# Kernel tuning notes

Measured on AMD Instinct MI355X. Metric: run time of the kernel, lower is better.

## Reference

```python
import jax, jax.numpy as jnp
import numpy as np

N = 50000       # num entities (nodes)
E = 800000      # num edges
R = 200         # num relation types
DIN = 64        # dim_in_ent
DREL = 64       # dim_rel
DOUT = 64       # dim_out_ent
H = 8           # num_head
DH = DOUT // H  # dim_hid_ent
EPS = 1e-6


def setup_inputs() -> dict:
    key = jax.random.key(0)
    ks = jax.random.split(key, 8)
    return {
        "emb_ent": jax.random.normal(ks[0], (N, DIN), dtype=jnp.float32),
        "emb_rel": jax.random.normal(ks[1], (R, DREL), dtype=jnp.float32),
        "attn_W": jax.random.normal(ks[2], (DOUT, 2 * DIN + DREL), dtype=jnp.float32) * 0.05,
        "attn_b": jnp.zeros((DOUT,), dtype=jnp.float32),
        "attn_vec": jax.random.normal(ks[3], (1, H, DH), dtype=jnp.float32) * 0.05,
        "aggr_W": jax.random.normal(ks[4], (DOUT, DIN + DREL), dtype=jnp.float32) * 0.05,
        "aggr_b": jnp.zeros((DOUT,), dtype=jnp.float32),
        "head_idxs": jax.random.randint(ks[5], (E,), 0, N),
        "tail_idxs": jax.random.randint(ks[6], (E,), 0, N),
        "rel_idxs": jax.random.randint(ks[7], (E,), 0, R),
    }


def reference(emb_ent, emb_rel, attn_W, attn_b, attn_vec, aggr_W, aggr_b,
              head_idxs, tail_idxs, rel_idxs):
    num_ent = emb_ent.shape[0]
    # per-node in-degree and mean incoming relation embedding (self relation)
    ones = jnp.ones(tail_idxs.shape[0], dtype=emb_ent.dtype)
    ent_freq = jax.ops.segment_sum(ones, tail_idxs, num_segments=num_ent)[:, None]
    rel_e = emb_rel[rel_idxs]                                             # [E, DREL]
    self_rel = jax.ops.segment_sum(rel_e, tail_idxs, num_segments=num_ent) / (ent_freq + EPS)
    # append self-loops: every node gets a self edge carrying self_rel
    emb_rels = jnp.concatenate([rel_e, self_rel], axis=0)                 # [E+N, DREL]
    sl = jnp.arange(num_ent)
    h_idx = jnp.concatenate([head_idxs, sl], axis=0)                      # [M]
    t_idx = jnp.concatenate([tail_idxs, sl], axis=0)                      # [M]
    # attention logits per edge per head
    cat_att = jnp.concatenate([emb_ent[t_idx], emb_ent[h_idx], emb_rels], axis=-1)  # [M, 2*DIN+DREL]
    a = jax.nn.leaky_relu(cat_att @ attn_W.T + attn_b, negative_slope=0.2)
    a = a.reshape(-1, H, DH)
    raw = jnp.sum(a * attn_vec, axis=-1)                                  # [M, H]
    # per-destination-node multi-head softmax (stable, segment-wise)
    mx = jax.ops.segment_max(raw, t_idx, num_segments=num_ent)            # [num_ent, H]
    mx = jnp.where(jnp.isfinite(mx), mx, jnp.zeros_like(mx))              # empty segments -> 0 (matches torch init)
    av = jnp.exp(raw - mx[t_idx])                                         # [M, H]
    sums = jax.ops.segment_sum(av, t_idx, num_segments=num_ent)           # [num_ent, H]
    beta = av / (sums[t_idx] + EPS)                                       # [M, H]
    # message projection and weighted scatter-add aggregation
    cat = jnp.concatenate([emb_ent[h_idx], emb_rels], axis=-1)            # [M, DIN+DREL]
    aggr = (cat @ aggr_W.T + aggr_b).reshape(-1, H, DH)                   # [M, H, DH]
    out = jax.ops.segment_sum(beta[..., None] * aggr, t_idx, num_segments=num_ent)  # [num_ent, H, DH]
    return out.reshape(num_ent, H * DH)
```

## Files before the change

### kernel.cpp

```cpp
#include <hip/hip_runtime.h>
#include <math.h>

#define EPS 1e-6f

typedef _Float16 half2v __attribute__((ext_vector_type(2)));

__device__ __forceinline__ unsigned f2bf(float x) {
    unsigned u = __float_as_uint(x);
    return (u + 0x7FFFu + ((u >> 16) & 1u)) >> 16;
}

__device__ __forceinline__ float dpp_add_xor1(float t) {
    int u = __builtin_amdgcn_update_dpp(0, __float_as_int(t), 0xB1, 0xF, 0xF, true);
    return t + __int_as_float(u);
}
__device__ __forceinline__ float dpp_add_xor2(float t) {
    int u = __builtin_amdgcn_update_dpp(0, __float_as_int(t), 0x4E, 0xF, 0xF, true);
    return t + __int_as_float(u);
}
__device__ __forceinline__ float dpp_add_mirr8(float t) {
    int u = __builtin_amdgcn_update_dpp(0, __float_as_int(t), 0x141, 0xF, 0xF, true);
    return t + __int_as_float(u);
}

__device__ __forceinline__ float fdot2u(unsigned a, unsigned b, float c) {
    return __builtin_amdgcn_fdot2(__builtin_bit_cast(half2v, a),
                                  __builtin_bit_cast(half2v, b), c, false);
}
__device__ __forceinline__ unsigned pk16(float x, float y) {
    return __builtin_bit_cast(unsigned, __builtin_amdgcn_cvt_pkrtz(x, y));
}

__global__ __launch_bounds__(256) void tables_hist(
    const float* __restrict__ A, int M,
    const float* __restrict__ Ar, int Mr,
    const float* __restrict__ attn_W,
    const float* __restrict__ aggr_W,
    const float* __restrict__ attn_b, const float* __restrict__ aggr_b,
    float* __restrict__ Pt,
    unsigned short* __restrict__ PQh2,
    unsigned short* __restrict__ PQr2,
    const int* __restrict__ tail, int E, int* __restrict__ deg,
    int gN, int gr)
{
    __shared__ alignas(16) unsigned short As16[64][72];
    __shared__ alignas(16) unsigned short Ws16[64][72];
    const int tid = threadIdx.x;
    const int bid = (int)blockIdx.x;
    const int nEnt = 3 * gN;
    const int nRel = 2 * gr;

    if (bid < nEnt + nRel) {
        int slice, rt, Mrows;
        const float* Asrc;
        if (bid < nEnt) { slice = bid / gN;     rt = bid % gN; Asrc = A;  Mrows = M;  }
        else { int b2 = bid - nEnt; slice = 3 + b2 / gr; rt = b2 % gr; Asrc = Ar; Mrows = Mr; }
        const int r0 = rt * 64;

        for (int t = tid; t < 1024; t += 256) {
            int r = t >> 4, c4 = (t & 15) << 2;
            float4 v = make_float4(0.f, 0.f, 0.f, 0.f);
            if (r0 + r < Mrows)
                v = *reinterpret_cast<const float4*>(Asrc + (size_t)(r0 + r) * 64 + c4);
            *reinterpret_cast<uint2*>(&As16[r][c4]) =
                make_uint2(pk16(v.x, v.y), pk16(v.z, v.w));
        }
        const float* Wsrc; int ldw, koff;
        switch (slice) {
        case 0:  Wsrc = attn_W; ldw = 192; koff = 0;   break;
        case 1:  Wsrc = attn_W; ldw = 192; koff = 64;  break;
        case 2:  Wsrc = aggr_W; ldw = 128; koff = 0;   break;
        case 3:  Wsrc = attn_W; ldw = 192; koff = 128; break;
        default: Wsrc = aggr_W; ldw = 128; koff = 64;  break;
        }
        for (int t = tid; t < 1024; t += 256) {
            int c = t >> 4, k4 = (t & 15) << 2;
            float4 v = *reinterpret_cast<const float4*>(
                Wsrc + (size_t)c * ldw + koff + k4);
            *reinterpret_cast<uint2*>(&Ws16[c][k4]) =
                make_uint2(pk16(v.x, v.y), pk16(v.z, v.w));
        }
        __syncthreads();

        const int ti = tid >> 4, tj = tid & 15;
        float acc[4][4];
#pragma unroll
        for (int i = 0; i < 4; ++i)
#pragma unroll
            for (int j = 0; j < 4; ++j) acc[i][j] = 0.f;

#pragma unroll
        for (int k = 0; k < 64; k += 8) {
            uint4 a8[4], w8[4];
#pragma unroll
            for (int i = 0; i < 4; ++i)
                a8[i] = *reinterpret_cast<const uint4*>(&As16[ti + 16 * i][k]);
#pragma unroll
            for (int j = 0; j < 4; ++j)
                w8[j] = *reinterpret_cast<const uint4*>(&Ws16[tj + 16 * j][k]);
#pragma unroll
            for (int i = 0; i < 4; ++i)
#pragma unroll
                for (int j = 0; j < 4; ++j) {
                    float c0 = acc[i][j];
                    c0 = fdot2u(a8[i].x, w8[j].x, c0);
                    c0 = fdot2u(a8[i].y, w8[j].y, c0);
                    c0 = fdot2u(a8[i].z, w8[j].z, c0);
                    c0 = fdot2u(a8[i].w, w8[j].w, c0);
                    acc[i][j] = c0;
                }
        }

        if (slice == 0) {
#pragma unroll
            for (int i = 0; i < 4; ++i) {
                int r = r0 + ti + 16 * i;
                if (r < M)
#pragma unroll
                    for (int j = 0; j < 4; ++j)
                        Pt[(size_t)r * 64 + tj + 16 * j] = acc[i][j];
            }
        } else if (slice == 1) {
#pragma unroll
            for (int i = 0; i < 4; ++i) {
                int r = r0 + ti + 16 * i;
                if (r < M)
#pragma unroll
                    for (int j = 0; j < 4; ++j) {
                        int c = tj + 16 * j;
                        PQh2[((size_t)r * 64 + c) * 2 + 0] =
                            (unsigned short)f2bf(acc[i][j] + attn_b[c]);
                    }
            }
        } else if (slice == 2) {
#pragma unroll
            for (int i = 0; i < 4; ++i) {
                int r = r0 + ti + 16 * i;
                if (r < M)
#pragma unroll
                    for (int j = 0; j < 4; ++j) {
                        int c = tj + 16 * j;
                        PQh2[((size_t)r * 64 + c) * 2 + 1] =
                            (unsigned short)f2bf(acc[i][j] + aggr_b[c]);
                    }
            }
        } else if (slice == 3) {
#pragma unroll
            for (int i = 0; i < 4; ++i) {
                int r = r0 + ti + 16 * i;
                if (r < Mr)
#pragma unroll
                    for (int j = 0; j < 4; ++j)
                        PQr2[((size_t)r * 64 + tj + 16 * j) * 2 + 0] =
                            (unsigned short)f2bf(acc[i][j]);
            }
        } else {
#pragma unroll
            for (int i = 0; i < 4; ++i) {
                int r = r0 + ti + 16 * i;
                if (r < Mr)
#pragma unroll
                    for (int j = 0; j < 4; ++j)
                        PQr2[((size_t)r * 64 + tj + 16 * j) * 2 + 1] =
                            (unsigned short)f2bf(acc[i][j]);
            }
        }
    } else {
        const int base = ((bid - nEnt - nRel) * 256 + tid) * 4;
        if (base + 4 <= E) {
            int4 t4 = *reinterpret_cast<const int4*>(tail + base);
            atomicAdd(&deg[t4.x], 1);
            atomicAdd(&deg[t4.y], 1);
            atomicAdd(&deg[t4.z], 1);
            atomicAdd(&deg[t4.w], 1);
        } else {
            for (int k = 0; k < 4; ++k)
                if (base + k < E) atomicAdd(&deg[tail[base + k]], 1);
        }
    }
}

__global__ __launch_bounds__(256) void scan_chunk(const int* __restrict__ deg, int n,
                                                  int* __restrict__ incl, int* __restrict__ bsums)
{
    __shared__ int s[256];
    int tid = threadIdx.x;
    int i = blockIdx.x * 256 + tid;
    int v = (i < n) ? deg[i] : 0;
    int acc = v;
    s[tid] = acc;
    __syncthreads();
#pragma unroll
    for (int off = 1; off < 256; off <<= 1) {
        int add = (tid >= off) ? s[tid - off] : 0;
        __syncthreads();
        acc += add;
        s[tid] = acc;
        __syncthreads();
    }
    if (i < n) incl[i] = acc;
    if (tid == 255) bsums[blockIdx.x] = acc;
}

__global__ __launch_bounds__(256) void scan_final2(const int* __restrict__ deg,
                                                   const int* __restrict__ incl,
                                                   const int* __restrict__ bsums, int n,
                                                   int* __restrict__ offs,
                                                   int* __restrict__ cursor)
{
    __shared__ int s[256];
    const int tid = threadIdx.x;
    int partial = 0;
    for (int i = tid; i < (int)blockIdx.x; i += 256) partial += bsums[i];
    s[tid] = partial;
    __syncthreads();
#pragma unroll
    for (int off = 128; off > 0; off >>= 1) {
        if (tid < off) s[tid] += s[tid + off];
        __syncthreads();
    }
    const int base = s[0];
    int i = blockIdx.x * 256 + tid;
    if (i < n) {
        int e = incl[i] - deg[i] + base;
        offs[i] = e;
        cursor[i] = e;
    }
}

__global__ __launch_bounds__(256) void place_kernel(const int* __restrict__ head,
                                                    const int* __restrict__ tail,
                                                    const int* __restrict__ rel, int E,
                                                    int* __restrict__ cursor,
                                                    unsigned int* __restrict__ shr)
{
    const int base = (blockIdx.x * 256 + threadIdx.x) * 4;
    if (base + 4 <= E) {
        int4 h = *reinterpret_cast<const int4*>(head + base);
        int4 t = *reinterpret_cast<const int4*>(tail + base);
        int4 r = *reinterpret_cast<const int4*>(rel + base);
        int p;
        p = atomicAdd(&cursor[t.x], 1); shr[p] = ((unsigned)h.x << 8) | (unsigned)r.x;
        p = atomicAdd(&cursor[t.y], 1); shr[p] = ((unsigned)h.y << 8) | (unsigned)r.y;
        p = atomicAdd(&cursor[t.z], 1); shr[p] = ((unsigned)h.z << 8) | (unsigned)r.z;
        p = atomicAdd(&cursor[t.w], 1); shr[p] = ((unsigned)h.w << 8) | (unsigned)r.w;
    } else {
        for (int k = 0; k < 4; ++k) {
            int e = base + k;
            if (e < E) {
                int p = atomicAdd(&cursor[tail[e]], 1);
                shr[p] = ((unsigned)head[e] << 8) | (unsigned)rel[e];
            }
        }
    }
}

__global__ __launch_bounds__(256) void ingram_main(
    const float* __restrict__ Pt,
    const unsigned* __restrict__ PQh,
    const unsigned* __restrict__ PQr,
    const int* __restrict__ deg, const int* __restrict__ off,
    const unsigned* __restrict__ shr,
    const float* __restrict__ attn_vec,
    float* __restrict__ out, int N)
{
    const int lane = threadIdx.x & 63;
    const int node = blockIdx.x * 4 + (threadIdx.x >> 6);
    if (node >= N) return;

    const float vec = attn_vec[lane];
    const float ptd = Pt[(size_t)node * 64 + lane];
    const char* HBc = (const char*)PQh;
    const char* RBc = (const char*)PQr;
    const unsigned loff4 = (unsigned)lane << 2;

    const int start = __builtin_amdgcn_readfirstlane(off[node]);
    const int dg    = __builtin_amdgcn_readfirstlane(deg[node]);

    float S = 0.f, O = 0.f, SP = 0.f, SQ = 0.f;

    const int ng = (dg + 7) >> 3;
    unsigned Ah[8], Ar8[8], Bh[8], Br8[8];

#define LOADG(gbase, H, R)                                                   \
    {                                                                        \
        _Pragma("unroll")                                                    \
        for (int k = 0; k < 8; ++k) {                                        \
            int idx = (gbase) + k;                                           \
            int e   = start + ((idx < dg) ? idx : (dg - 1));                 \
            unsigned p = shr[e];            \
            H[k] = *(const unsigned*)(HBc + (p & 0xFFFFFF00u) + loff4);      \
            R[k] = *(const unsigned*)(RBc + ((p & 255u) << 8) + loff4);      \
        }                                                                    \
    }

#define COMPUTE(gbase, H, R)                                                 \
    {                                                                        \
        _Pragma("unroll")                                                    \
        for (int k = 0; k < 8; ++k) {                                        \
            const int idx = (gbase) + k;                                     \
            const float valid = (idx < dg) ? 1.f : 0.f;                      \
            unsigned hb = H[k], rb = R[k];                                   \
            float hx = __uint_as_float(hb << 16);                            \
            float hy = __uint_as_float(hb & 0xFFFF0000u);                    \
            float rx = __uint_as_float(rb << 16);                            \
            float ry = __uint_as_float(rb & 0xFFFF0000u);                    \
            SP = fmaf(rx, valid, SP);                                        \
            SQ = fmaf(ry, valid, SQ);                                        \
            float pre = ptd + hx + rx;                                       \
            float a   = fmaxf(pre, 0.2f * pre);                              \
            float t   = a * vec;                                             \
            t = dpp_add_xor1(t);                                             \
            t = dpp_add_xor2(t);                                             \
            t = dpp_add_mirr8(t);                                            \
            float av = __expf(t) * valid;                                    \
            S += av;                                                         \
            O = fmaf(av, hy + ry, O);                                        \
        }                                                                    \
    }

    if (ng > 0) LOADG(0, Ah, Ar8);
    for (int g = 0; g < ng; g += 2) {
        if (g + 1 < ng) LOADG((g + 1) * 8, Bh, Br8);
        COMPUTE(g * 8, Ah, Ar8);
        if (g + 1 < ng) {
            if (g + 2 < ng) LOADG((g + 2) * 8, Ah, Ar8);
            COMPUTE((g + 1) * 8, Bh, Br8);
        }
    }
#undef LOADG
#undef COMPUTE

    {
        const float inv = 1.f / ((float)dg + EPS);
        unsigned hb = *(const unsigned*)(HBc + ((unsigned)node << 8) + loff4);
        float hx = __uint_as_float(hb << 16);
        float hy = __uint_as_float(hb & 0xFFFF0000u);
        float pre = ptd + hx + SP * inv;
        float a   = fmaxf(pre, 0.2f * pre);
        float t   = a * vec;
        t = dpp_add_xor1(t);
        t = dpp_add_xor2(t);
        t = dpp_add_mirr8(t);
        float av = __expf(t);
        S += av;
        O = fmaf(av, hy + SQ * inv, O);
    }

    out[(size_t)node * 64 + lane] = O / (S + EPS);
}

extern "C" void kernel_launch(void* const* d_in, const int* in_sizes, int n_in,
                              void* d_out, int out_size, void* d_ws, size_t ws_size,
                              hipStream_t stream)
{
    const float* emb_ent  = (const float*)d_in[0];
    const float* emb_rel  = (const float*)d_in[1];
    const float* attn_W   = (const float*)d_in[2];
    const float* attn_b   = (const float*)d_in[3];
    const float* attn_vec = (const float*)d_in[4];
    const float* aggr_W   = (const float*)d_in[5];
    const float* aggr_b   = (const float*)d_in[6];
    const int*   head     = (const int*)d_in[7];
    const int*   tail     = (const int*)d_in[8];
    const int*   rel      = (const int*)d_in[9];

    const int N = in_sizes[0] / 64;
    const int R = in_sizes[1] / 64;
    const int E = in_sizes[7];

    char* w = (char*)d_ws;
    float*    Pt  = (float*)w;        w += (size_t)N * 64 * sizeof(float);
    unsigned* PQh = (unsigned*)w;     w += (size_t)N * 64 * sizeof(unsigned);
    unsigned* PQr = (unsigned*)w;     w += (size_t)R * 64 * sizeof(unsigned);
    int* deg    = (int*)w;            w += (size_t)N * sizeof(int);
    int* incl   = (int*)w;            w += (size_t)N * sizeof(int);
    int* offs   = (int*)w;            w += (size_t)N * sizeof(int);
    int* cursor = (int*)w;            w += (size_t)N * sizeof(int);
    int* bsums  = (int*)w;            w += 256 * sizeof(int);
    unsigned int* shr = (unsigned int*)w;  w += (size_t)E * sizeof(unsigned int);

    hipMemsetAsync(deg, 0, (size_t)N * sizeof(int), stream);

    int gN = (N + 63) / 64;
    int gr = (R + 63) / 64;
    int gH = (E + 1023) / 1024;
    tables_hist<<<3 * gN + 2 * gr + gH, 256, 0, stream>>>(
        emb_ent, N, emb_rel, R, attn_W, aggr_W, attn_b, aggr_b,
        Pt, (unsigned short*)PQh, (unsigned short*)PQr,
        tail, E, deg, gN, gr);

    int nb = (N + 255) / 256;
    scan_chunk<<<nb, 256, 0, stream>>>(deg, N, incl, bsums);
    scan_final2<<<nb, 256, 0, stream>>>(deg, incl, bsums, N, offs, cursor);
    place_kernel<<<(E + 1023) / 1024, 256, 0, stream>>>(head, tail, rel, E, cursor, shr);

    ingram_main<<<(N + 3) / 4, 256, 0, stream>>>(Pt, PQh, PQr, deg, offs, shr,
                                                 attn_vec, (float*)d_out, N);
}
```

Baseline: 156.8 us.

## Fuse CSR construction into one cooperative kernel with grid-wide syncs

Replaces the memset, histogram, two scan kernels and placement kernel with a single cooperative kernel that zeroes degrees, builds the histogram, scans and places edges, separated by grid.sync barriers. The scan now has each block sum all preceding degrees directly instead of using a block-sums pass. The table GEMM moves into its own kernel and no longer overlaps with the histogram. This removes several launch gaps. In exchange it adds grid-barrier cost, a redundant O(N) prefix read per block, and a cooperative launch that requires all 2048 blocks to be co-resident.

```diff
diff --git a/kernel.cpp b/kernel.cpp
--- a/kernel.cpp
+++ b/kernel.cpp
@@ -1,5 +1,8 @@
 #include <hip/hip_runtime.h>
+#include <hip/hip_cooperative_groups.h>
 #include <math.h>
+
+namespace cg = cooperative_groups;
 
 #define EPS 1e-6f
 
@@ -31,142 +34,23 @@
     return __builtin_bit_cast(unsigned, __builtin_amdgcn_cvt_pkrtz(x, y));
 }
 
-__global__ __launch_bounds__(256) void tables_hist(
-    const float* __restrict__ A, int M,
-    const float* __restrict__ Ar, int Mr,
-    const float* __restrict__ attn_W,
-    const float* __restrict__ aggr_W,
-    const float* __restrict__ attn_b, const float* __restrict__ aggr_b,
-    float* __restrict__ Pt,
-    unsigned short* __restrict__ PQh2,
-    unsigned short* __restrict__ PQr2,
-    const int* __restrict__ tail, int E, int* __restrict__ deg,
-    int gN, int gr)
+__global__ __launch_bounds__(256) void csr_coop(
+    const int* __restrict__ head, const int* __restrict__ tail,
+    const int* __restrict__ rel, int E, int N,
+    int* __restrict__ deg, int* __restrict__ offs,
+    int* __restrict__ cursor, unsigned* __restrict__ shr)
 {
-    __shared__ alignas(16) unsigned short As16[64][72];
-    __shared__ alignas(16) unsigned short Ws16[64][72];
-    const int tid = threadIdx.x;
-    const int bid = (int)blockIdx.x;
-    const int nEnt = 3 * gN;
-    const int nRel = 2 * gr;
-
-    if (bid < nEnt + nRel) {
-        int slice, rt, Mrows;
-        const float* Asrc;
-        if (bid < nEnt) { slice = bid / gN;     rt = bid % gN; Asrc = A;  Mrows = M;  }
-        else { int b2 = bid - nEnt; slice = 3 + b2 / gr; rt = b2 % gr; Asrc = Ar; Mrows = Mr; }
-        const int r0 = rt * 64;
-
-        for (int t = tid; t < 1024; t += 256) {
-            int r = t >> 4, c4 = (t & 15) << 2;
-            float4 v = make_float4(0.f, 0.f, 0.f, 0.f);
-            if (r0 + r < Mrows)
-                v = *reinterpret_cast<const float4*>(Asrc + (size_t)(r0 + r) * 64 + c4);
-            *reinterpret_cast<uint2*>(&As16[r][c4]) =
-                make_uint2(pk16(v.x, v.y), pk16(v.z, v.w));
-        }
-        const float* Wsrc; int ldw, koff;
-        switch (slice) {
-        case 0:  Wsrc = attn_W; ldw = 192; koff = 0;   break;
-        case 1:  Wsrc = attn_W; ldw = 192; koff = 64;  break;
-        case 2:  Wsrc = aggr_W; ldw = 128; koff = 0;   break;
-        case 3:  Wsrc = attn_W; ldw = 192; koff = 128; break;
-        default: Wsrc = aggr_W; ldw = 128; koff = 64;  break;
-        }
-        for (int t = tid; t < 1024; t += 256) {
-            int c = t >> 4, k4 = (t & 15) << 2;
-            float4 v = *reinterpret_cast<const float4*>(
-                Wsrc + (size_t)c * ldw + koff + k4);
-            *reinterpret_cast<uint2*>(&Ws16[c][k4]) =
-                make_uint2(pk16(v.x, v.y), pk16(v.z, v.w));
-        }
-        __syncthreads();
-
-        const int ti = tid >> 4, tj = tid & 15;
-        float acc[4][4];
-#pragma unroll
-        for (int i = 0; i < 4; ++i)
-#pragma unroll
-            for (int j = 0; j < 4; ++j) acc[i][j] = 0.f;
-
-#pragma unroll
-        for (int k = 0; k < 64; k += 8) {
-            uint4 a8[4], w8[4];
-#pragma unroll
-            for (int i = 0; i < 4; ++i)
-                a8[i] = *reinterpret_cast<const uint4*>(&As16[ti + 16 * i][k]);
-#pragma unroll
-            for (int j = 0; j < 4; ++j)
-                w8[j] = *reinterpret_cast<const uint4*>(&Ws16[tj + 16 * j][k]);
-#pragma unroll
-            for (int i = 0; i < 4; ++i)
-#pragma unroll
-                for (int j = 0; j < 4; ++j) {
-                    float c0 = acc[i][j];
-                    c0 = fdot2u(a8[i].x, w8[j].x, c0);
-                    c0 = fdot2u(a8[i].y, w8[j].y, c0);
-                    c0 = fdot2u(a8[i].z, w8[j].z, c0);
-                    c0 = fdot2u(a8[i].w, w8[j].w, c0);
-                    acc[i][j] = c0;
-                }
-        }
-
-        if (slice == 0) {
-#pragma unroll
-            for (int i = 0; i < 4; ++i) {
-                int r = r0 + ti + 16 * i;
-                if (r < M)
-#pragma unroll
-                    for (int j = 0; j < 4; ++j)
-                        Pt[(size_t)r * 64 + tj + 16 * j] = acc[i][j];
-            }
-        } else if (slice == 1) {
-#pragma unroll
-            for (int i = 0; i < 4; ++i) {
-                int r = r0 + ti + 16 * i;
-                if (r < M)
-#pragma unroll
-                    for (int j = 0; j < 4; ++j) {
-                        int c = tj + 16 * j;
-                        PQh2[((size_t)r * 64 + c) * 2 + 0] =
-                            (unsigned short)f2bf(acc[i][j] + attn_b[c]);
-                    }
-            }
-        } else if (slice == 2) {
-#pragma unroll
-            for (int i = 0; i < 4; ++i) {
-                int r = r0 + ti + 16 * i;
-                if (r < M)
-#pragma unroll
-                    for (int j = 0; j < 4; ++j) {
-                        int c = tj + 16 * j;
-                        PQh2[((size_t)r * 64 + c) * 2 + 1] =
-                            (unsigned short)f2bf(acc[i][j] + aggr_b[c]);
-                    }
-            }
-        } else if (slice == 3) {
-#pragma unroll
-            for (int i = 0; i < 4; ++i) {
-                int r = r0 + ti + 16 * i;
-                if (r < Mr)
-#pragma unroll
-                    for (int j = 0; j < 4; ++j)
-                        PQr2[((size_t)r * 64 + tj + 16 * j) * 2 + 0] =
-                            (unsigned short)f2bf(acc[i][j]);
-            }
-        } else {
-#pragma unroll
-            for (int i = 0; i < 4; ++i) {
-                int r = r0 + ti + 16 * i;
-                if (r < Mr)
-#pragma unroll
-                    for (int j = 0; j < 4; ++j)
-                        PQr2[((size_t)r * 64 + tj + 16 * j) * 2 + 1] =
-                            (unsigned short)f2bf(acc[i][j]);
-            }
-        }
-    } else {
-        const int base = ((bid - nEnt - nRel) * 256 + tid) * 4;
+    cg::grid_group grid = cg::this_grid();
+    __shared__ int s[256];
+    __shared__ int sb[256];
+    const int tid  = threadIdx.x;
+    const int gtid = (int)blockIdx.x * 256 + tid;
+    const int gsz  = (int)gridDim.x * 256;
+
+    for (int i = gtid; i < N; i += gsz) deg[i] = 0;
+    grid.sync();
+
+    for (int base = gtid * 4; base < E; base += gsz * 4) {
         if (base + 4 <= E) {
             int4 t4 = *reinterpret_cast<const int4*>(tail + base);
             atomicAdd(&deg[t4.x], 1);
@@ -178,79 +62,194 @@
                 if (base + k < E) atomicAdd(&deg[tail[base + k]], 1);
         }
     }
-}
-
-__global__ __launch_bounds__(256) void scan_chunk(const int* __restrict__ deg, int n,
-                                                  int* __restrict__ incl, int* __restrict__ bsums)
-{
-    __shared__ int s[256];
-    int tid = threadIdx.x;
-    int i = blockIdx.x * 256 + tid;
-    int v = (i < n) ? deg[i] : 0;
-    int acc = v;
-    s[tid] = acc;
-    __syncthreads();
-#pragma unroll
-    for (int off = 1; off < 256; off <<= 1) {
-        int add = (tid >= off) ? s[tid - off] : 0;
+    grid.sync();
+
+    const int nb = (N + 255) / 256;
+    if ((int)blockIdx.x < nb) {
+        const int limit = (int)blockIdx.x * 256;
+        int partial = 0;
+        for (int i = tid; i < limit; i += 256) partial += deg[i];
+        sb[tid] = partial;
         __syncthreads();
-        acc += add;
+#pragma unroll
+        for (int off = 128; off > 0; off >>= 1) {
+            if (tid < off) sb[tid] += sb[tid + off];
+            __syncthreads();
+        }
+        const int base = sb[0];
+
+        const int i = limit + tid;
+        const int v = (i < N) ? deg[i] : 0;
+        int acc = v;
         s[tid] = acc;
         __syncthreads();
-    }
-    if (i < n) incl[i] = acc;
-    if (tid == 255) bsums[blockIdx.x] = acc;
-}
-
-__global__ __launch_bounds__(256) void scan_final2(const int* __restrict__ deg,
-                                                   const int* __restrict__ incl,
-                                                   const int* __restrict__ bsums, int n,
-                                                   int* __restrict__ offs,
-                                                   int* __restrict__ cursor)
+#pragma unroll
+        for (int off = 1; off < 256; off <<= 1) {
+            int add = (tid >= off) ? s[tid - off] : 0;
+            __syncthreads();
+            acc += add;
+            s[tid] = acc;
+            __syncthreads();
+        }
+        if (i < N) {
+            int e = base + acc - v;
+            offs[i] = e;
+            cursor[i] = e;
+        }
+    }
+    grid.sync();
+
+    for (int base = gtid * 4; base < E; base += gsz * 4) {
+        if (base + 4 <= E) {
+            int4 h = *reinterpret_cast<const int4*>(head + base);
+            int4 t = *reinterpret_cast<const int4*>(tail + base);
+            int4 r = *reinterpret_cast<const int4*>(rel + base);
+            int p;
+            p = atomicAdd(&cursor[t.x], 1); shr[p] = ((unsigned)h.x << 8) | (unsigned)r.x;
+            p = atomicAdd(&cursor[t.y], 1); shr[p] = ((unsigned)h.y << 8) | (unsigned)r.y;
+            p = atomicAdd(&cursor[t.z], 1); shr[p] = ((unsigned)h.z << 8) | (unsigned)r.z;
+            p = atomicAdd(&cursor[t.w], 1); shr[p] = ((unsigned)h.w << 8) | (unsigned)r.w;
+        } else {
+            for (int k = 0; k < 4; ++k) {
+                int e = base + k;
+                if (e < E) {
+                    int p = atomicAdd(&cursor[tail[e]], 1);
+                    shr[p] = ((unsigned)head[e] << 8) | (unsigned)rel[e];
+                }
+            }
+        }
+    }
+}
+
+__global__ __launch_bounds__(256) void tables_kernel(
+    const float* __restrict__ A, int M,
+    const float* __restrict__ Ar, int Mr,
+    const float* __restrict__ attn_W,
+    const float* __restrict__ aggr_W,
+    const float* __restrict__ attn_b, const float* __restrict__ aggr_b,
+    float* __restrict__ Pt,
+    unsigned short* __restrict__ PQh2,
+    unsigned short* __restrict__ PQr2,
+    int gN, int gr)
 {
-    __shared__ int s[256];
+    __shared__ alignas(16) unsigned short As16[64][72];
+    __shared__ alignas(16) unsigned short Ws16[64][72];
     const int tid = threadIdx.x;
-    int partial = 0;
-    for (int i = tid; i < (int)blockIdx.x; i += 256) partial += bsums[i];
-    s[tid] = partial;
+    const int bid = (int)blockIdx.x;
+    const int nEnt = 3 * gN;
+
+    int slice, rt, Mrows;
+    const float* Asrc;
+    if (bid < nEnt) { slice = bid / gN;     rt = bid % gN; Asrc = A;  Mrows = M;  }
+    else { int b2 = bid - nEnt; slice = 3 + b2 / gr; rt = b2 % gr; Asrc = Ar; Mrows = Mr; }
+    const int r0 = rt * 64;
+
+    for (int t = tid; t < 1024; t += 256) {
+        int r = t >> 4, c4 = (t & 15) << 2;
+        float4 v = make_float4(0.f, 0.f, 0.f, 0.f);
+        if (r0 + r < Mrows)
+            v = *reinterpret_cast<const float4*>(Asrc + (size_t)(r0 + r) * 64 + c4);
+        *reinterpret_cast<uint2*>(&As16[r][c4]) =
+            make_uint2(pk16(v.x, v.y), pk16(v.z, v.w));
+    }
+    const float* Wsrc; int ldw, koff;
+    switch (slice) {
+    case 0:  Wsrc = attn_W; ldw = 192; koff = 0;   break;
+    case 1:  Wsrc = attn_W; ldw = 192; koff = 64;  break;
+    case 2:  Wsrc = aggr_W; ldw = 128; koff = 0;   break;
+    case 3:  Wsrc = attn_W; ldw = 192; koff = 128; break;
+    default: Wsrc = aggr_W; ldw = 128; koff = 64;  break;
+    }
+    for (int t = tid; t < 1024; t += 256) {
+        int c = t >> 4, k4 = (t & 15) << 2;
+        float4 v = *reinterpret_cast<const float4*>(
+            Wsrc + (size_t)c * ldw + koff + k4);
+        *reinterpret_cast<uint2*>(&Ws16[c][k4]) =
+            make_uint2(pk16(v.x, v.y), pk16(v.z, v.w));
+    }
     __syncthreads();
-#pragma unroll
-    for (int off = 128; off > 0; off >>= 1) {
-        if (tid < off) s[tid] += s[tid + off];
-        __syncthreads();
-    }
-    const int base = s[0];
-    int i = blockIdx.x * 256 + tid;
-    if (i < n) {
-        int e = incl[i] - deg[i] + base;
-        offs[i] = e;
-        cursor[i] = e;
-    }
-}
-
-__global__ __launch_bounds__(256) void place_kernel(const int* __restrict__ head,
-                                                    const int* __restrict__ tail,
-                                                    const int* __restrict__ rel, int E,
-                                                    int* __restrict__ cursor,
-                                                    unsigned int* __restrict__ shr)
-{
-    const int base = (blockIdx.x * 256 + threadIdx.x) * 4;
-    if (base + 4 <= E) {
-        int4 h = *reinterpret_cast<const int4*>(head + base);
-        int4 t = *reinterpret_cast<const int4*>(tail + base);
-        int4 r = *reinterpret_cast<const int4*>(rel + base);
-        int p;
-        p = atomicAdd(&cursor[t.x], 1); shr[p] = ((unsigned)h.x << 8) | (unsigned)r.x;
-        p = atomicAdd(&cursor[t.y], 1); shr[p] = ((unsigned)h.y << 8) | (unsigned)r.y;
-        p = atomicAdd(&cursor[t.z], 1); shr[p] = ((unsigned)h.z << 8) | (unsigned)r.z;
-        p = atomicAdd(&cursor[t.w], 1); shr[p] = ((unsigned)h.w << 8) | (unsigned)r.w;
+
+    const int ti = tid >> 4, tj = tid & 15;
+    float acc[4][4];
+#pragma unroll
+    for (int i = 0; i < 4; ++i)
+#pragma unroll
+        for (int j = 0; j < 4; ++j) acc[i][j] = 0.f;
+
+#pragma unroll
+    for (int k = 0; k < 64; k += 8) {
+        uint4 a8[4], w8[4];
+#pragma unroll
+        for (int i = 0; i < 4; ++i)
+            a8[i] = *reinterpret_cast<const uint4*>(&As16[ti + 16 * i][k]);
+#pragma unroll
+        for (int j = 0; j < 4; ++j)
+            w8[j] = *reinterpret_cast<const uint4*>(&Ws16[tj + 16 * j][k]);
+#pragma unroll
+        for (int i = 0; i < 4; ++i)
+#pragma unroll
+            for (int j = 0; j < 4; ++j) {
+                float c0 = acc[i][j];
+                c0 = fdot2u(a8[i].x, w8[j].x, c0);
+                c0 = fdot2u(a8[i].y, w8[j].y, c0);
+                c0 = fdot2u(a8[i].z, w8[j].z, c0);
+                c0 = fdot2u(a8[i].w, w8[j].w, c0);
+                acc[i][j] = c0;
+            }
+    }
+
+    if (slice == 0) {
+#pragma unroll
+        for (int i = 0; i < 4; ++i) {
+            int r = r0 + ti + 16 * i;
+            if (r < M)
+#pragma unroll
+                for (int j = 0; j < 4; ++j)
+                    Pt[(size_t)r * 64 + tj + 16 * j] = acc[i][j];
+        }
+    } else if (slice == 1) {
+#pragma unroll
+        for (int i = 0; i < 4; ++i) {
+            int r = r0 + ti + 16 * i;
+            if (r < M)
+#pragma unroll
+                for (int j = 0; j < 4; ++j) {
+                    int c = tj + 16 * j;
+                    PQh2[((size_t)r * 64 + c) * 2 + 0] =
+                        (unsigned short)f2bf(acc[i][j] + attn_b[c]);
+                }
+        }
+    } else if (slice == 2) {
+#pragma unroll
+        for (int i = 0; i < 4; ++i) {
+            int r = r0 + ti + 16 * i;
+            if (r < M)
+#pragma unroll
+                for (int j = 0; j < 4; ++j) {
+                    int c = tj + 16 * j;
+                    PQh2[((size_t)r * 64 + c) * 2 + 1] =
+                        (unsigned short)f2bf(acc[i][j] + aggr_b[c]);
+                }
+        }
+    } else if (slice == 3) {
+#pragma unroll
+        for (int i = 0; i < 4; ++i) {
+            int r = r0 + ti + 16 * i;
+            if (r < Mr)
+#pragma unroll
+                for (int j = 0; j < 4; ++j)
+                    PQr2[((size_t)r * 64 + tj + 16 * j) * 2 + 0] =
+                        (unsigned short)f2bf(acc[i][j]);
+        }
     } else {
-        for (int k = 0; k < 4; ++k) {
-            int e = base + k;
-            if (e < E) {
-                int p = atomicAdd(&cursor[tail[e]], 1);
-                shr[p] = ((unsigned)head[e] << 8) | (unsigned)rel[e];
-            }
+#pragma unroll
+        for (int i = 0; i < 4; ++i) {
+            int r = r0 + ti + 16 * i;
+            if (r < Mr)
+#pragma unroll
+                for (int j = 0; j < 4; ++j)
+                    PQr2[((size_t)r * 64 + tj + 16 * j) * 2 + 1] =
+                        (unsigned short)f2bf(acc[i][j]);
         }
     }
 }
@@ -365,35 +364,36 @@
     const int*   tail     = (const int*)d_in[8];
     const int*   rel      = (const int*)d_in[9];
 
-    const int N = in_sizes[0] / 64;
-    const int R = in_sizes[1] / 64;
-    const int E = in_sizes[7];
+    int N = in_sizes[0] / 64;
+    int R = in_sizes[1] / 64;
+    int E = in_sizes[7];
 
     char* w = (char*)d_ws;
     float*    Pt  = (float*)w;        w += (size_t)N * 64 * sizeof(float);
     unsigned* PQh = (unsigned*)w;     w += (size_t)N * 64 * sizeof(unsigned);
     unsigned* PQr = (unsigned*)w;     w += (size_t)R * 64 * sizeof(unsigned);
     int* deg    = (int*)w;            w += (size_t)N * sizeof(int);
-    int* incl   = (int*)w;            w += (size_t)N * sizeof(int);
     int* offs   = (int*)w;            w += (size_t)N * sizeof(int);
     int* cursor = (int*)w;            w += (size_t)N * sizeof(int);
-    int* bsums  = (int*)w;            w += 256 * sizeof(int);
-    unsigned int* shr = (unsigned int*)w;  w += (size_t)E * sizeof(unsigned int);
-
-    hipMemsetAsync(deg, 0, (size_t)N * sizeof(int), stream);
+    unsigned* shr = (unsigned*)w;     w += (size_t)E * sizeof(unsigned);
+
+    int gC = (E + 1023) / 1024;
+    if (gC > 2048) gC = 2048;
+    if (gC < 1) gC = 1;
+    {
+        void* cargs[] = { (void*)&head, (void*)&tail, (void*)&rel,
+                          (void*)&E, (void*)&N,
+                          (void*)&deg, (void*)&offs, (void*)&cursor,
+                          (void*)&shr };
+        hipLaunchCooperativeKernel((void*)csr_coop, dim3(gC), dim3(256),
+                                   cargs, 0, stream);
+    }
 
     int gN = (N + 63) / 64;
     int gr = (R + 63) / 64;
-    int gH = (E + 1023) / 1024;
-    tables_hist<<<3 * gN + 2 * gr + gH, 256, 0, stream>>>(
+    tables_kernel<<<3 * gN + 2 * gr, 256, 0, stream>>>(
         emb_ent, N, emb_rel, R, attn_W, aggr_W, attn_b, aggr_b,
-        Pt, (unsigned short*)PQh, (unsigned short*)PQr,
-        tail, E, deg, gN, gr);
-
-    int nb = (N + 255) / 256;
-    scan_chunk<<<nb, 256, 0, stream>>>(deg, N, incl, bsums);
-    scan_final2<<<nb, 256, 0, stream>>>(deg, incl, bsums, N, offs, cursor);
-    place_kernel<<<(E + 1023) / 1024, 256, 0, stream>>>(head, tail, rel, E, cursor, shr);
+        Pt, (unsigned short*)PQh, (unsigned short*)PQr, gN, gr);
 
     ingram_main<<<(N + 3) / 4, 256, 0, stream>>>(Pt, PQh, PQr, deg, offs, shr,
                                                  attn_vec, (float*)d_out, N);
```

Measured after the change: 397.7 us. 2.54x slower.
